# Kernel tuning notes

Hardware: AMD Instinct MI355X
Metric: run time of the kernel (lower is better)

The kernel has to match this reference:

```python
import jax, jax.numpy as jnp
import numpy as np

C_M, C_Z, C = 256, 128, 32
N_SEQ, N_RES = 128, 256


def setup_inputs() -> dict:
    key = jax.random.key(0)
    ks = jax.random.split(key, 9)
    s = 0.02
    return {
        "m": jax.random.normal(ks[0], (N_SEQ, N_RES, C_M), dtype=jnp.float32),
        "ln_w": jnp.ones((C_M,), dtype=jnp.float32),
        "ln_b": jnp.zeros((C_M,), dtype=jnp.float32),
        "w1": jax.random.normal(ks[1], (C, C_M), dtype=jnp.float32) * s,
        "b1": jnp.zeros((C,), dtype=jnp.float32),
        "w2": jax.random.normal(ks[2], (C, C_M), dtype=jnp.float32) * s,
        "b2": jnp.zeros((C,), dtype=jnp.float32),
        "wo": jax.random.normal(ks[3], (C_Z, C * C), dtype=jnp.float32) * s,
        "bo": jnp.zeros((C_Z,), dtype=jnp.float32),
    }


def reference(m, ln_w, ln_b, w1, b1, w2, b2, wo, bo):
    n_seq = m.shape[-3]
    # LayerNorm over c_m
    mu = jnp.mean(m, axis=-1, keepdims=True)
    var = jnp.mean(jnp.square(m - mu), axis=-1, keepdims=True)
    mn = (m - mu) * jax.lax.rsqrt(var + 1e-5) * ln_w + ln_b
    # dual projections to c channels: [s, i, c]
    a = jnp.einsum('sim,cm->sic', mn, w1) + b1
    b = jnp.einsum('sjm,dm->sjd', mn, w2) + b2
    # outer product mean contracted over sequence axis: [i, j, c, d]
    o = jnp.einsum('sic,sjd->ijcd', a, b)
    o = o.reshape(o.shape[0], o.shape[1], C * C)
    # output projection and mean over sequences
    z = (jnp.einsum('ijk,zk->ijz', o, wo) + bo) / n_seq
    return z
```

## Files before the change

### kernel.cpp

```cpp
#include <hip/hip_runtime.h>
#include <hip/hip_bf16.h>
#include <stdint.h>

#define N_RES 256
#define CMDIM 256

typedef __attribute__((ext_vector_type(8))) short bf16x8;
typedef __attribute__((ext_vector_type(4))) float f32x4;
typedef __attribute__((ext_vector_type(2))) unsigned int u32x2;

__device__ __forceinline__ unsigned short f32_to_bf16(float f) {
    union { float f; unsigned int u; } v; v.f = f;
    unsigned int u = v.u;
    return (unsigned short)((u + 0x7FFFu + ((u >> 16) & 1u)) >> 16);
}


__global__ __launch_bounds__(256) void k_prep(
    const float* __restrict__ w1, const float* __restrict__ w2,
    const float* __restrict__ wo,
    unsigned short* __restrict__ Wbf, unsigned short* __restrict__ wof)
{
    int t = blockIdx.x * 256 + threadIdx.x;
    if (t < 16384) {
        int ch = t >> 8, cm = t & 255;
        float v = (ch < 32) ? w1[ch * 256 + cm] : w2[(ch - 32) * 256 + cm];
        int addr = ((ch >> 4) * 8 + (cm >> 5)) * 512 + ((cm >> 3) & 3) * 128 + (ch & 15) * 8 + (cm & 7);
        Wbf[addr] = f32_to_bf16(v);
    }
    if (t < 131072) {
        int zo = t >> 10, k = t & 1023;
        int addr = ((zo >> 4) * 32 + (k >> 5)) * 512 + ((k >> 3) & 3) * 128 + (zo & 15) * 8 + (k & 7);
        wof[addr] = f32_to_bf16(wo[t]);
    }
}

__global__ __launch_bounds__(256) void k_ln_proj(
    const float* __restrict__ m, const float* __restrict__ lnw, const float* __restrict__ lnb,
    const float* __restrict__ b1, const float* __restrict__ b2,
    const unsigned short* __restrict__ Wbf,
    unsigned short* __restrict__ A2f, unsigned short* __restrict__ B2f)
{
    __shared__ unsigned short mn[32 * 256];
    __shared__ unsigned short stg[2048];
    int b = blockIdx.x;
    int i = b >> 2, sblk = b & 3;
    int tid = threadIdx.x;
    int wv = tid >> 6, lane = tid & 63;
    int quad = lane >> 4, l15 = lane & 15;

    f32x4 lw = *(const f32x4*)(lnw + lane * 4);
    f32x4 lb = *(const f32x4*)(lnb + lane * 4);

    #pragma unroll
    for (int r = 0; r < 8; ++r) {
        int sl = wv * 8 + r;
        int s = sblk * 32 + sl;
        const float* row = m + ((size_t)s * N_RES + i) * CMDIM;
        f32x4 x = *(const f32x4*)(row + lane * 4);
        float s1 = x[0] + x[1] + x[2] + x[3];
        float s2 = x[0]*x[0] + x[1]*x[1] + x[2]*x[2] + x[3]*x[3];
        #pragma unroll
        for (int off = 32; off; off >>= 1) {
            s1 += __shfl_xor(s1, off);
            s2 += __shfl_xor(s2, off);
        }
        float mu = s1 * (1.0f / 256.0f);
        float var = s2 * (1.0f / 256.0f) - mu * mu;
        float rstd = rsqrtf(var + 1e-5f);
        float n0 = (x[0] - mu) * rstd * lw[0] + lb[0];
        float n1 = (x[1] - mu) * rstd * lw[1] + lb[1];
        float n2 = (x[2] - mu) * rstd * lw[2] + lb[2];
        float n3 = (x[3] - mu) * rstd * lw[3] + lb[3];
        unsigned int p0 = (unsigned)f32_to_bf16(n0) | ((unsigned)f32_to_bf16(n1) << 16);
        unsigned int p1 = (unsigned)f32_to_bf16(n2) | ((unsigned)f32_to_bf16(n3) << 16);
        int chunk = lane >> 1;
        int pos = (chunk & 16) | ((chunk ^ sl) & 15);
        unsigned int* dst = (unsigned int*)((char*)mn + sl * 512 + pos * 16 + (lane & 1) * 8);
        dst[0] = p0; dst[1] = p1;
    }
    __syncthreads();

    bf16x8 af[8];
    #pragma unroll
    for (int ks = 0; ks < 8; ++ks)
        af[ks] = *(const bf16x8*)(Wbf + (wv * 8 + ks) * 512 + lane * 8);

    f32x4 acc[2];
    acc[0] = (f32x4){0.f, 0.f, 0.f, 0.f};
    acc[1] = (f32x4){0.f, 0.f, 0.f, 0.f};
    #pragma unroll
    for (int ks = 0; ks < 8; ++ks) {
        #pragma unroll
        for (int nb = 0; nb < 2; ++nb) {
            int sl = nb * 16 + l15;
            int chunk = ks * 4 + quad;
            int pos = (chunk & 16) | ((chunk ^ sl) & 15);
            bf16x8 bf = *(const bf16x8*)((char*)mn + sl * 512 + pos * 16);
            acc[nb] = __builtin_amdgcn_mfma_f32_16x16x32_bf16(af[ks], bf, acc[nb], 0, 0, 0);
        }
    }

    const float* bsrc = (wv < 2) ? b1 : b2;
    f32x4 bias = *(const f32x4*)(bsrc + (wv & 1) * 16 + quad * 4);
    unsigned short* sbase = stg + (wv >> 1) * 1024 + (wv & 1) * 512 + quad * 32;
    #pragma unroll
    for (int nb = 0; nb < 2; ++nb) {
        int sl = nb * 16 + l15;
        int soff = ((sl >> 3) & 3) * 128 + (sl & 7);
        #pragma unroll
        for (int reg = 0; reg < 4; ++reg)
            sbase[soff + reg * 8] = f32_to_bf16(acc[nb][reg] + bias[reg]);
    }
    __syncthreads();

    int part = tid >> 7, blk = (tid >> 6) & 1, l = tid & 63;
    unsigned short* gdst = (part ? B2f : A2f) + ((i * 2 + blk) * 4 + sblk) * 512 + l * 8;
    *(bf16x8*)gdst = *(const bf16x8*)(stg + tid * 8);
}

__global__ __launch_bounds__(256, 2) void k_fused(
    const unsigned short* __restrict__ A2f, const unsigned short* __restrict__ B2f,
    const unsigned short* __restrict__ wof, const float* __restrict__ bo,
    float* __restrict__ out)
{
    __shared__ char olds[65536];
    int bx = blockIdx.x;
    int by = blockIdx.y;
    int tid = threadIdx.x, wv = tid >> 6, lane = tid & 63;
    int quad = lane >> 4, l15 = lane & 15;
    int wm = wv & 1, wn = wv >> 1;

    bf16x8 bn[4][4];
    #pragma unroll
    for (int ks = 0; ks < 4; ++ks)
        #pragma unroll
        for (int nb = 0; nb < 4; ++nb)
            bn[ks][nb] = *(const bf16x8*)(A2f + (size_t)(((bx * 8 + wn * 4 + nb) * 4 + ks) * 512) + lane * 8);

    #pragma unroll
    for (int pass = 0; pass < 2; ++pass) {
        f32x4 acc[4][4];
        #pragma unroll
        for (int a = 0; a < 4; ++a)
            #pragma unroll
            for (int b = 0; b < 4; ++b) acc[a][b] = (f32x4){0.f, 0.f, 0.f, 0.f};

        bf16x8 amC[4], amN[4];
        #pragma unroll
        for (int mb = 0; mb < 4; ++mb)
            amC[mb] = *(const bf16x8*)(B2f + (size_t)(((by * 16 + pass * 8 + wm * 4 + mb) * 4 + 0) * 512) + lane * 8);

        #pragma unroll
        for (int ks = 0; ks < 4; ++ks) {
            if (ks < 3) {
                #pragma unroll
                for (int mb = 0; mb < 4; ++mb)
                    amN[mb] = *(const bf16x8*)(B2f + (size_t)(((by * 16 + pass * 8 + wm * 4 + mb) * 4 + ks + 1) * 512) + lane * 8);
            }
            #pragma unroll
            for (int mb = 0; mb < 4; ++mb)
                #pragma unroll
                for (int nb = 0; nb < 4; ++nb)
                    acc[mb][nb] = __builtin_amdgcn_mfma_f32_16x16x32_bf16(amC[mb], bn[ks][nb], acc[mb][nb], 0, 0, 0);
            #pragma unroll
            for (int mb = 0; mb < 4; ++mb) amC[mb] = amN[mb];
        }

        #pragma unroll
        for (int mb = 0; mb < 4; ++mb) {
            int m_ = wm * 64 + mb * 16 + quad * 4;
            int d0 = m_ & 31;
            int jl = pass * 4 + (m_ >> 5);
            #pragma unroll
            for (int nb = 0; nb < 4; ++nb) {
                int n_ = wn * 64 + nb * 16 + l15;
                int c = n_ & 31, il = n_ >> 5;
                int pair = il * 8 + jl;
                int e0 = c * 32 + d0;
                int chunk = e0 >> 3;
                int phys = pair ^ (chunk & 31);
                f32x4 a4 = acc[mb][nb];
                unsigned int p0 = (unsigned)f32_to_bf16(a4[0]) | ((unsigned)f32_to_bf16(a4[1]) << 16);
                unsigned int p1 = (unsigned)f32_to_bf16(a4[2]) | ((unsigned)f32_to_bf16(a4[3]) << 16);
                u32x2 pv = {p0, p1};
                *(u32x2*)(olds + chunk * 512 + phys * 16 + (e0 & 7) * 2) = pv;
            }
        }
    }
    __syncthreads();

    f32x4 acc2[2][2];
    #pragma unroll
    for (int a = 0; a < 2; ++a)
        #pragma unroll
        for (int b = 0; b < 2; ++b) acc2[a][b] = (f32x4){0.f, 0.f, 0.f, 0.f};

    const unsigned short* wbase = wof + (size_t)(wv * 2 * 32) * 512 + lane * 8;

    bf16x8 af[4][2], bfr[4][2];
    #pragma unroll
    for (int p = 0; p < 3; ++p) {
        #pragma unroll
        for (int zb = 0; zb < 2; ++zb)
            af[p][zb] = *(const bf16x8*)(wbase + (size_t)(zb * 32 + p) * 512);
        #pragma unroll
        for (int pb = 0; pb < 2; ++pb) {
            int pair = pb * 16 + l15;
            int chunk = p * 4 + quad;
            int phys = pair ^ (chunk & 31);
            bfr[p][pb] = *(const bf16x8*)(olds + chunk * 512 + phys * 16);
        }
    }

    #pragma unroll
    for (int kt = 0; kt < 32; ++kt) {
        int slot = kt & 3;
        if (kt + 3 < 32) {
            int pf = kt + 3, ps = pf & 3;
            #pragma unroll
            for (int zb = 0; zb < 2; ++zb)
                af[ps][zb] = *(const bf16x8*)(wbase + (size_t)(zb * 32 + pf) * 512);
            #pragma unroll
            for (int pb = 0; pb < 2; ++pb) {
                int pair = pb * 16 + l15;
                int chunk = pf * 4 + quad;
                int phys = pair ^ (chunk & 31);
                bfr[ps][pb] = *(const bf16x8*)(olds + chunk * 512 + phys * 16);
            }
        }
        #pragma unroll
        for (int zb = 0; zb < 2; ++zb)
            #pragma unroll
            for (int pb = 0; pb < 2; ++pb)
                acc2[zb][pb] = __builtin_amdgcn_mfma_f32_16x16x32_bf16(af[slot][zb], bfr[slot][pb], acc2[zb][pb], 0, 0, 0);
    }

    #pragma unroll
    for (int zb = 0; zb < 2; ++zb) {
        int zo = wv * 32 + zb * 16 + quad * 4;
        f32x4 b4 = *(const f32x4*)(bo + zo);
        #pragma unroll
        for (int pb = 0; pb < 2; ++pb) {
            int pair = pb * 16 + l15;
            int i = bx * 4 + (pair >> 3);
            int j = by * 8 + (pair & 7);
            f32x4 v;
            #pragma unroll
            for (int reg = 0; reg < 4; ++reg)
                v[reg] = (acc2[zb][pb][reg] + b4[reg]) * (1.0f / 128.0f);
            *(f32x4*)(out + ((size_t)(i * 256 + j)) * 128 + zo) = v;
        }
    }
}

extern "C" void kernel_launch(void* const* d_in, const int* in_sizes, int n_in,
                              void* d_out, int out_size, void* d_ws, size_t ws_size,
                              hipStream_t stream) {
    const float* m   = (const float*)d_in[0];
    const float* lnw = (const float*)d_in[1];
    const float* lnb = (const float*)d_in[2];
    const float* w1  = (const float*)d_in[3];
    const float* b1  = (const float*)d_in[4];
    const float* w2  = (const float*)d_in[5];
    const float* b2  = (const float*)d_in[6];
    const float* wo  = (const float*)d_in[7];
    const float* bo  = (const float*)d_in[8];
    float* out = (float*)d_out;
    char* ws = (char*)d_ws;

    unsigned short* Wbf = (unsigned short*)(ws);
    unsigned short* wof = (unsigned short*)(ws + 32768);
    unsigned short* A2f = (unsigned short*)(ws + 32768 + 262144);
    unsigned short* B2f = (unsigned short*)(ws + 32768 + 262144 + 2097152);

    hipLaunchKernelGGL(k_prep, dim3(512), dim3(256), 0, stream, w1, w2, wo, Wbf, wof);
    hipLaunchKernelGGL(k_ln_proj, dim3(1024), dim3(256), 0, stream,
                       m, lnw, lnb, b1, b2, Wbf, A2f, B2f);
    hipLaunchKernelGGL(k_fused, dim3(64, 32), dim3(256), 0, stream,
                       A2f, B2f, wof, bo, out);
}
```

Measured before the change: 139.0 us.

## Double fused tile to 8x8 residue pairs with 512-thread blocks

The fused outer-product plus projection kernel now processes 64 (i,j) pairs per block (8 i by 8 j) using 8 waves and 128KB of LDS, instead of 32 pairs with 4 waves. The first GEMM is done in a single pass with 8x4 MFMA tiles per wave, and weight prefetch for the output projection is hoisted above the barrier. This halves the grid and gives better reuse of A/B fragments and wo loads per block. In exchange, occupancy drops to one block per CU because of the LDS size, and register pressure rises from the 32 accumulators.

```diff
diff --git a/kernel.cpp b/kernel.cpp
--- a/kernel.cpp
+++ b/kernel.cpp
@@ -119,99 +119,104 @@
     *(bf16x8*)gdst = *(const bf16x8*)(stg + tid * 8);
 }
 
-__global__ __launch_bounds__(256, 2) void k_fused(
+__global__ __launch_bounds__(512) void k_fused(
     const unsigned short* __restrict__ A2f, const unsigned short* __restrict__ B2f,
     const unsigned short* __restrict__ wof, const float* __restrict__ bo,
     float* __restrict__ out)
 {
-    __shared__ char olds[65536];
+    __shared__ char olds[131072];
     int bx = blockIdx.x;
     int by = blockIdx.y;
     int tid = threadIdx.x, wv = tid >> 6, lane = tid & 63;
     int quad = lane >> 4, l15 = lane & 15;
-    int wm = wv & 1, wn = wv >> 1;
-
-    bf16x8 bn[4][4];
-    #pragma unroll
-    for (int ks = 0; ks < 4; ++ks)
-        #pragma unroll
-        for (int nb = 0; nb < 4; ++nb)
-            bn[ks][nb] = *(const bf16x8*)(A2f + (size_t)(((bx * 8 + wn * 4 + nb) * 4 + ks) * 512) + lane * 8);
-
-    #pragma unroll
-    for (int pass = 0; pass < 2; ++pass) {
-        f32x4 acc[4][4];
-        #pragma unroll
-        for (int a = 0; a < 4; ++a)
-            #pragma unroll
-            for (int b = 0; b < 4; ++b) acc[a][b] = (f32x4){0.f, 0.f, 0.f, 0.f};
-
-        bf16x8 amC[4], amN[4];
-        #pragma unroll
-        for (int mb = 0; mb < 4; ++mb)
-            amC[mb] = *(const bf16x8*)(B2f + (size_t)(((by * 16 + pass * 8 + wm * 4 + mb) * 4 + 0) * 512) + lane * 8);
-
-        #pragma unroll
-        for (int ks = 0; ks < 4; ++ks) {
-            if (ks < 3) {
-                #pragma unroll
-                for (int mb = 0; mb < 4; ++mb)
-                    amN[mb] = *(const bf16x8*)(B2f + (size_t)(((by * 16 + pass * 8 + wm * 4 + mb) * 4 + ks + 1) * 512) + lane * 8);
-            }
-            #pragma unroll
-            for (int mb = 0; mb < 4; ++mb)
-                #pragma unroll
-                for (int nb = 0; nb < 4; ++nb)
-                    acc[mb][nb] = __builtin_amdgcn_mfma_f32_16x16x32_bf16(amC[mb], bn[ks][nb], acc[mb][nb], 0, 0, 0);
-            #pragma unroll
-            for (int mb = 0; mb < 4; ++mb) amC[mb] = amN[mb];
-        }
-
-        #pragma unroll
-        for (int mb = 0; mb < 4; ++mb) {
-            int m_ = wm * 64 + mb * 16 + quad * 4;
-            int d0 = m_ & 31;
-            int jl = pass * 4 + (m_ >> 5);
-            #pragma unroll
-            for (int nb = 0; nb < 4; ++nb) {
-                int n_ = wn * 64 + nb * 16 + l15;
-                int c = n_ & 31, il = n_ >> 5;
-                int pair = il * 8 + jl;
-                int e0 = c * 32 + d0;
-                int chunk = e0 >> 3;
-                int phys = pair ^ (chunk & 31);
-                f32x4 a4 = acc[mb][nb];
-                unsigned int p0 = (unsigned)f32_to_bf16(a4[0]) | ((unsigned)f32_to_bf16(a4[1]) << 16);
-                unsigned int p1 = (unsigned)f32_to_bf16(a4[2]) | ((unsigned)f32_to_bf16(a4[3]) << 16);
-                u32x2 pv = {p0, p1};
-                *(u32x2*)(olds + chunk * 512 + phys * 16 + (e0 & 7) * 2) = pv;
-            }
-        }
-    }
+    int wm = wv & 1, wn = wv >> 2 == 0 ? (wv >> 1) : (wv >> 1);
+    wn = wv >> 1;
+
+    const unsigned short* Abase = A2f + (size_t)((bx * 16 + wn * 4) * 4) * 512 + lane * 8;
+    const unsigned short* Bbase = B2f + (size_t)((by * 16 + wm * 8) * 4) * 512 + lane * 8;
+
+    f32x4 acc[8][4];
+    #pragma unroll
+    for (int a = 0; a < 8; ++a)
+        #pragma unroll
+        for (int b = 0; b < 4; ++b) acc[a][b] = (f32x4){0.f, 0.f, 0.f, 0.f};
+
+    bf16x8 amC[8], amN[8], bnC[4], bnN[4];
+    #pragma unroll
+    for (int mb = 0; mb < 8; ++mb)
+        amC[mb] = *(const bf16x8*)(Bbase + (size_t)(mb * 4) * 512);
+    #pragma unroll
+    for (int nb = 0; nb < 4; ++nb)
+        bnC[nb] = *(const bf16x8*)(Abase + (size_t)(nb * 4) * 512);
+
+    #pragma unroll
+    for (int ks = 0; ks < 4; ++ks) {
+        if (ks < 3) {
+            #pragma unroll
+            for (int mb = 0; mb < 8; ++mb)
+                amN[mb] = *(const bf16x8*)(Bbase + (size_t)(mb * 4 + ks + 1) * 512);
+            #pragma unroll
+            for (int nb = 0; nb < 4; ++nb)
+                bnN[nb] = *(const bf16x8*)(Abase + (size_t)(nb * 4 + ks + 1) * 512);
+        }
+        #pragma unroll
+        for (int mb = 0; mb < 8; ++mb)
+            #pragma unroll
+            for (int nb = 0; nb < 4; ++nb)
+                acc[mb][nb] = __builtin_amdgcn_mfma_f32_16x16x32_bf16(amC[mb], bnC[nb], acc[mb][nb], 0, 0, 0);
+        #pragma unroll
+        for (int mb = 0; mb < 8; ++mb) amC[mb] = amN[mb];
+        #pragma unroll
+        for (int nb = 0; nb < 4; ++nb) bnC[nb] = bnN[nb];
+    }
+
+    #pragma unroll
+    for (int mb = 0; mb < 8; ++mb) {
+        int d0 = (mb & 1) * 16 + quad * 4;
+        int jl = wm * 4 + (mb >> 1);
+        #pragma unroll
+        for (int nb = 0; nb < 4; ++nb) {
+            int c = (nb & 1) * 16 + l15;
+            int il = wn * 2 + (nb >> 1);
+            int pair = il * 8 + jl;
+            int e0 = c * 32 + d0;
+            int chunk = e0 >> 3;
+            int phys = pair ^ (chunk & 63);
+            f32x4 a4 = acc[mb][nb];
+            unsigned int p0 = (unsigned)f32_to_bf16(a4[0]) | ((unsigned)f32_to_bf16(a4[1]) << 16);
+            unsigned int p1 = (unsigned)f32_to_bf16(a4[2]) | ((unsigned)f32_to_bf16(a4[3]) << 16);
+            u32x2 pv = {p0, p1};
+            *(u32x2*)(olds + chunk * 1024 + phys * 16 + (quad & 1) * 8) = pv;
+        }
+    }
+
+    int zg = wv >> 1, pg = wv & 1;
+    const unsigned short* wbase = wof + (size_t)(zg * 64) * 512 + lane * 8;
+
+    bf16x8 af2[4][2], bfr[4][2];
+    #pragma unroll
+    for (int p = 0; p < 3; ++p)
+        #pragma unroll
+        for (int zb = 0; zb < 2; ++zb)
+            af2[p][zb] = *(const bf16x8*)(wbase + (size_t)(zb * 32 + p) * 512);
+
     __syncthreads();
 
+    #pragma unroll
+    for (int p = 0; p < 3; ++p)
+        #pragma unroll
+        for (int pb = 0; pb < 2; ++pb) {
+            int pair = pg * 32 + pb * 16 + l15;
+            int chunk = p * 4 + quad;
+            int phys = pair ^ (chunk & 63);
+            bfr[p][pb] = *(const bf16x8*)(olds + chunk * 1024 + phys * 16);
+        }
+
     f32x4 acc2[2][2];
     #pragma unroll
     for (int a = 0; a < 2; ++a)
         #pragma unroll
         for (int b = 0; b < 2; ++b) acc2[a][b] = (f32x4){0.f, 0.f, 0.f, 0.f};
-
-    const unsigned short* wbase = wof + (size_t)(wv * 2 * 32) * 512 + lane * 8;
-
-    bf16x8 af[4][2], bfr[4][2];
-    #pragma unroll
-    for (int p = 0; p < 3; ++p) {
-        #pragma unroll
-        for (int zb = 0; zb < 2; ++zb)
-            af[p][zb] = *(const bf16x8*)(wbase + (size_t)(zb * 32 + p) * 512);
-        #pragma unroll
-        for (int pb = 0; pb < 2; ++pb) {
-            int pair = pb * 16 + l15;
-            int chunk = p * 4 + quad;
-            int phys = pair ^ (chunk & 31);
-            bfr[p][pb] = *(const bf16x8*)(olds + chunk * 512 + phys * 16);
-        }
-    }
 
     #pragma unroll
     for (int kt = 0; kt < 32; ++kt) {
@@ -220,30 +225,30 @@
             int pf = kt + 3, ps = pf & 3;
             #pragma unroll
             for (int zb = 0; zb < 2; ++zb)
-                af[ps][zb] = *(const bf16x8*)(wbase + (size_t)(zb * 32 + pf) * 512);
+                af2[ps][zb] = *(const bf16x8*)(wbase + (size_t)(zb * 32 + pf) * 512);
             #pragma unroll
             for (int pb = 0; pb < 2; ++pb) {
-                int pair = pb * 16 + l15;
+                int pair = pg * 32 + pb * 16 + l15;
                 int chunk = pf * 4 + quad;
-                int phys = pair ^ (chunk & 31);
-                bfr[ps][pb] = *(const bf16x8*)(olds + chunk * 512 + phys * 16);
+                int phys = pair ^ (chunk & 63);
+                bfr[ps][pb] = *(const bf16x8*)(olds + chunk * 1024 + phys * 16);
             }
         }
         #pragma unroll
         for (int zb = 0; zb < 2; ++zb)
             #pragma unroll
             for (int pb = 0; pb < 2; ++pb)
-                acc2[zb][pb] = __builtin_amdgcn_mfma_f32_16x16x32_bf16(af[slot][zb], bfr[slot][pb], acc2[zb][pb], 0, 0, 0);
+                acc2[zb][pb] = __builtin_amdgcn_mfma_f32_16x16x32_bf16(af2[slot][zb], bfr[slot][pb], acc2[zb][pb], 0, 0, 0);
     }
 
     #pragma unroll
     for (int zb = 0; zb < 2; ++zb) {
-        int zo = wv * 32 + zb * 16 + quad * 4;
+        int zo = zg * 32 + zb * 16 + quad * 4;
         f32x4 b4 = *(const f32x4*)(bo + zo);
         #pragma unroll
         for (int pb = 0; pb < 2; ++pb) {
-            int pair = pb * 16 + l15;
-            int i = bx * 4 + (pair >> 3);
+            int pair = pg * 32 + pb * 16 + l15;
+            int i = bx * 8 + (pair >> 3);
             int j = by * 8 + (pair & 7);
             f32x4 v;
             #pragma unroll
@@ -277,6 +282,6 @@
     hipLaunchKernelGGL(k_prep, dim3(512), dim3(256), 0, stream, w1, w2, wo, Wbf, wof);
     hipLaunchKernelGGL(k_ln_proj, dim3(1024), dim3(256), 0, stream,
                        m, lnw, lnb, b1, b2, Wbf, A2f, B2f);
-    hipLaunchKernelGGL(k_fused, dim3(64, 32), dim3(256), 0, stream,
+    hipLaunchKernelGGL(k_fused, dim3(32, 32), dim3(512), 0, stream,
                        A2f, B2f, wof, bo, out);
 }
```

Result: slower. 147.2 us (+5.9%).

## Double fused tile to 8x8 pairs with 512 threads and split-K reduction

Applied to the files above, without the earlier changes.

The fused outer-product and projection kernel now runs 512-thread blocks, each covering 8x8 (i,j) pairs instead of 4x8. The LDS staging buffer doubles to 128KB and uses a new 6-bit swizzle. The output-projection K loop is split between wave pairs, with the partial sums reduced through LDS. A blockIdx remap groups neighbouring tiles for L2 locality. The aim is to halve how often the wo weights are re-read per pair and to raise MFMA reuse, at the cost of lower occupancy from the large LDS footprint and an extra reduction barrier.

```diff
diff --git a/kernel.cpp b/kernel.cpp
--- a/kernel.cpp
+++ b/kernel.cpp
@@ -13,6 +13,10 @@
     union { float f; unsigned int u; } v; v.f = f;
     unsigned int u = v.u;
     return (unsigned short)((u + 0x7FFFu + ((u >> 16) & 1u)) >> 16);
+}
+
+__device__ __forceinline__ int swz6(int x) {
+    return ((x >> 2) & 7) | (((x >> 5) & 1) << 3) | ((x & 3) << 4);
 }
 
 
@@ -119,27 +123,31 @@
     *(bf16x8*)gdst = *(const bf16x8*)(stg + tid * 8);
 }
 
-__global__ __launch_bounds__(256, 2) void k_fused(
+__global__ __launch_bounds__(512, 2) void k_fused(
     const unsigned short* __restrict__ A2f, const unsigned short* __restrict__ B2f,
     const unsigned short* __restrict__ wof, const float* __restrict__ bo,
     float* __restrict__ out)
 {
-    __shared__ char olds[65536];
-    int bx = blockIdx.x;
-    int by = blockIdx.y;
+    __shared__ char olds[131072];
+    int bid = blockIdx.x;
+    int sb = (bid & 7) * 128 + (bid >> 3);
+    int bx = sb & 31, by = sb >> 5;
     int tid = threadIdx.x, wv = tid >> 6, lane = tid & 63;
     int quad = lane >> 4, l15 = lane & 15;
     int wm = wv & 1, wn = wv >> 1;
 
+    const unsigned short* Abase = A2f + (size_t)((bx * 16 + wn * 4) * 4) * 512 + lane * 8;
+
     bf16x8 bn[4][4];
     #pragma unroll
-    for (int ks = 0; ks < 4; ++ks)
-        #pragma unroll
-        for (int nb = 0; nb < 4; ++nb)
-            bn[ks][nb] = *(const bf16x8*)(A2f + (size_t)(((bx * 8 + wn * 4 + nb) * 4 + ks) * 512) + lane * 8);
+    for (int nb = 0; nb < 4; ++nb)
+        #pragma unroll
+        for (int ks = 0; ks < 4; ++ks)
+            bn[ks][nb] = *(const bf16x8*)(Abase + (size_t)(nb * 4 + ks) * 512);
 
     #pragma unroll
     for (int pass = 0; pass < 2; ++pass) {
+        const unsigned short* Bbase = B2f + (size_t)((by * 16 + pass * 8 + wm * 4) * 4) * 512 + lane * 8;
         f32x4 acc[4][4];
         #pragma unroll
         for (int a = 0; a < 4; ++a)
@@ -149,14 +157,14 @@
         bf16x8 amC[4], amN[4];
         #pragma unroll
         for (int mb = 0; mb < 4; ++mb)
-            amC[mb] = *(const bf16x8*)(B2f + (size_t)(((by * 16 + pass * 8 + wm * 4 + mb) * 4 + 0) * 512) + lane * 8);
+            amC[mb] = *(const bf16x8*)(Bbase + (size_t)(mb * 4) * 512);
 
         #pragma unroll
         for (int ks = 0; ks < 4; ++ks) {
             if (ks < 3) {
                 #pragma unroll
                 for (int mb = 0; mb < 4; ++mb)
-                    amN[mb] = *(const bf16x8*)(B2f + (size_t)(((by * 16 + pass * 8 + wm * 4 + mb) * 4 + ks + 1) * 512) + lane * 8);
+                    amN[mb] = *(const bf16x8*)(Bbase + (size_t)(mb * 4 + ks + 1) * 512);
             }
             #pragma unroll
             for (int mb = 0; mb < 4; ++mb)
@@ -179,77 +187,94 @@
                 int pair = il * 8 + jl;
                 int e0 = c * 32 + d0;
                 int chunk = e0 >> 3;
-                int phys = pair ^ (chunk & 31);
+                int phys = pair ^ swz6(chunk & 63);
                 f32x4 a4 = acc[mb][nb];
                 unsigned int p0 = (unsigned)f32_to_bf16(a4[0]) | ((unsigned)f32_to_bf16(a4[1]) << 16);
                 unsigned int p1 = (unsigned)f32_to_bf16(a4[2]) | ((unsigned)f32_to_bf16(a4[3]) << 16);
                 u32x2 pv = {p0, p1};
-                *(u32x2*)(olds + chunk * 512 + phys * 16 + (e0 & 7) * 2) = pv;
+                *(u32x2*)(olds + chunk * 1024 + phys * 16 + (e0 & 7) * 2) = pv;
             }
         }
     }
-    __syncthreads();
-
-    f32x4 acc2[2][2];
+
+    int zg = wv >> 1, kh = wv & 1, kt0 = kh * 16;
+    const unsigned short* wbase = wof + (size_t)(zg * 64) * 512 + lane * 8;
+
+    bf16x8 af2[4][2], bfr[4][4];
+    #pragma unroll
+    for (int p = 0; p < 3; ++p)
+        #pragma unroll
+        for (int zb = 0; zb < 2; ++zb)
+            af2[p][zb] = *(const bf16x8*)(wbase + (size_t)(zb * 32 + kt0 + p) * 512);
+
+    __syncthreads();
+
+    #pragma unroll
+    for (int p = 0; p < 3; ++p)
+        #pragma unroll
+        for (int pb = 0; pb < 4; ++pb) {
+            int pair = pb * 16 + l15;
+            int chunk = (kt0 + p) * 4 + quad;
+            int phys = pair ^ swz6(chunk & 63);
+            bfr[p][pb] = *(const bf16x8*)(olds + chunk * 1024 + phys * 16);
+        }
+
+    f32x4 acc2[2][4];
     #pragma unroll
     for (int a = 0; a < 2; ++a)
         #pragma unroll
-        for (int b = 0; b < 2; ++b) acc2[a][b] = (f32x4){0.f, 0.f, 0.f, 0.f};
-
-    const unsigned short* wbase = wof + (size_t)(wv * 2 * 32) * 512 + lane * 8;
-
-    bf16x8 af[4][2], bfr[4][2];
-    #pragma unroll
-    for (int p = 0; p < 3; ++p) {
-        #pragma unroll
-        for (int zb = 0; zb < 2; ++zb)
-            af[p][zb] = *(const bf16x8*)(wbase + (size_t)(zb * 32 + p) * 512);
-        #pragma unroll
-        for (int pb = 0; pb < 2; ++pb) {
-            int pair = pb * 16 + l15;
-            int chunk = p * 4 + quad;
-            int phys = pair ^ (chunk & 31);
-            bfr[p][pb] = *(const bf16x8*)(olds + chunk * 512 + phys * 16);
-        }
-    }
-
-    #pragma unroll
-    for (int kt = 0; kt < 32; ++kt) {
+        for (int b = 0; b < 4; ++b) acc2[a][b] = (f32x4){0.f, 0.f, 0.f, 0.f};
+
+    #pragma unroll
+    for (int kt = 0; kt < 16; ++kt) {
         int slot = kt & 3;
-        if (kt + 3 < 32) {
-            int pf = kt + 3, ps = pf & 3;
+        if (kt < 13) {
+            int pf = kt0 + kt + 3, ps = (kt + 3) & 3;
             #pragma unroll
             for (int zb = 0; zb < 2; ++zb)
-                af[ps][zb] = *(const bf16x8*)(wbase + (size_t)(zb * 32 + pf) * 512);
-            #pragma unroll
-            for (int pb = 0; pb < 2; ++pb) {
+                af2[ps][zb] = *(const bf16x8*)(wbase + (size_t)(zb * 32 + pf) * 512);
+            #pragma unroll
+            for (int pb = 0; pb < 4; ++pb) {
                 int pair = pb * 16 + l15;
                 int chunk = pf * 4 + quad;
-                int phys = pair ^ (chunk & 31);
-                bfr[ps][pb] = *(const bf16x8*)(olds + chunk * 512 + phys * 16);
+                int phys = pair ^ swz6(chunk & 63);
+                bfr[ps][pb] = *(const bf16x8*)(olds + chunk * 1024 + phys * 16);
             }
         }
         #pragma unroll
         for (int zb = 0; zb < 2; ++zb)
             #pragma unroll
-            for (int pb = 0; pb < 2; ++pb)
-                acc2[zb][pb] = __builtin_amdgcn_mfma_f32_16x16x32_bf16(af[slot][zb], bfr[slot][pb], acc2[zb][pb], 0, 0, 0);
-    }
-
-    #pragma unroll
-    for (int zb = 0; zb < 2; ++zb) {
-        int zo = wv * 32 + zb * 16 + quad * 4;
-        f32x4 b4 = *(const f32x4*)(bo + zo);
-        #pragma unroll
-        for (int pb = 0; pb < 2; ++pb) {
-            int pair = pb * 16 + l15;
-            int i = bx * 4 + (pair >> 3);
-            int j = by * 8 + (pair & 7);
-            f32x4 v;
-            #pragma unroll
-            for (int reg = 0; reg < 4; ++reg)
-                v[reg] = (acc2[zb][pb][reg] + b4[reg]) * (1.0f / 128.0f);
-            *(f32x4*)(out + ((size_t)(i * 256 + j)) * 128 + zo) = v;
+            for (int pb = 0; pb < 4; ++pb)
+                acc2[zb][pb] = __builtin_amdgcn_mfma_f32_16x16x32_bf16(af2[slot][zb], bfr[slot][pb], acc2[zb][pb], 0, 0, 0);
+    }
+
+    __syncthreads();
+    f32x4* red = (f32x4*)olds;
+    if (kh == 1) {
+        #pragma unroll
+        for (int zb = 0; zb < 2; ++zb)
+            #pragma unroll
+            for (int pb = 0; pb < 4; ++pb)
+                red[(((zg * 2 + zb) * 4 + pb) << 6) + quad * 16 + l15] = acc2[zb][pb];
+    }
+    __syncthreads();
+    if (kh == 0) {
+        #pragma unroll
+        for (int zb = 0; zb < 2; ++zb) {
+            int zo = zg * 32 + zb * 16 + quad * 4;
+            f32x4 b4 = *(const f32x4*)(bo + zo);
+            #pragma unroll
+            for (int pb = 0; pb < 4; ++pb) {
+                f32x4 part = red[(((zg * 2 + zb) * 4 + pb) << 6) + quad * 16 + l15];
+                int pair = pb * 16 + l15;
+                int i = bx * 8 + (pair >> 3);
+                int j = by * 8 + (pair & 7);
+                f32x4 v;
+                #pragma unroll
+                for (int reg = 0; reg < 4; ++reg)
+                    v[reg] = (acc2[zb][pb][reg] + part[reg] + b4[reg]) * (1.0f / 128.0f);
+                *(f32x4*)(out + ((size_t)(i * 256 + j)) * 128 + zo) = v;
+            }
         }
     }
 }
@@ -277,6 +302,6 @@
     hipLaunchKernelGGL(k_prep, dim3(512), dim3(256), 0, stream, w1, w2, wo, Wbf, wof);
     hipLaunchKernelGGL(k_ln_proj, dim3(1024), dim3(256), 0, stream,
                        m, lnw, lnb, b1, b2, Wbf, A2f, B2f);
-    hipLaunchKernelGGL(k_fused, dim3(64, 32), dim3(256), 0, stream,
+    hipLaunchKernelGGL(k_fused, dim3(1024), dim3(512), 0, stream,
                        A2f, B2f, wof, bo, out);
 }
```

Measured after the change: 140.2 us. About the same (+0.9%).

## Remap fused-kernel blocks, preload operands, deepen prefetch, add MFMA priority and new swizzle

Applied to the files above, without the earlier changes.

The fused outer-product/projection kernel now uses a 1D grid, remapped so that consecutive blocks are spread across by-rows, likely to group blocks by XCD for better L2 reuse of A/B tiles. All B-operand k-slices are loaded up front instead of double-buffered, and the wo-projection prefetch is issued before the barrier with two k-steps per pipeline slot. s_setprio raises wave priority around the MFMA bursts, and a different XOR swizzle is used for the LDS staging buffer to cut bank conflicts. These changes raise register pressure, which could hurt occupancy under launch_bounds(256,2).

```diff
diff --git a/kernel.cpp b/kernel.cpp
--- a/kernel.cpp
+++ b/kernel.cpp
@@ -13,6 +13,10 @@
     union { float f; unsigned int u; } v; v.f = f;
     unsigned int u = v.u;
     return (unsigned short)((u + 0x7FFFu + ((u >> 16) & 1u)) >> 16);
+}
+
+__device__ __forceinline__ int swz5(int x) {
+    return ((x >> 2) & 7) | (((x >> 5) & 1) << 3) | ((x & 1) << 4);
 }
 
 
@@ -125,47 +129,47 @@
     float* __restrict__ out)
 {
     __shared__ char olds[65536];
-    int bx = blockIdx.x;
-    int by = blockIdx.y;
+    int bid = blockIdx.x;
+    int sb = (bid & 7) * 256 + (bid >> 3);
+    int bx = sb & 63, by = sb >> 6;
     int tid = threadIdx.x, wv = tid >> 6, lane = tid & 63;
     int quad = lane >> 4, l15 = lane & 15;
     int wm = wv & 1, wn = wv >> 1;
 
+    const unsigned short* Abase = A2f + (size_t)((bx * 8 + wn * 4) * 4) * 512 + lane * 8;
+
     bf16x8 bn[4][4];
     #pragma unroll
-    for (int ks = 0; ks < 4; ++ks)
-        #pragma unroll
-        for (int nb = 0; nb < 4; ++nb)
-            bn[ks][nb] = *(const bf16x8*)(A2f + (size_t)(((bx * 8 + wn * 4 + nb) * 4 + ks) * 512) + lane * 8);
+    for (int nb = 0; nb < 4; ++nb)
+        #pragma unroll
+        for (int ks = 0; ks < 4; ++ks)
+            bn[ks][nb] = *(const bf16x8*)(Abase + (size_t)(nb * 4 + ks) * 512);
 
     #pragma unroll
     for (int pass = 0; pass < 2; ++pass) {
+        const unsigned short* Bbase = B2f + (size_t)((by * 16 + pass * 8 + wm * 4) * 4) * 512 + lane * 8;
         f32x4 acc[4][4];
         #pragma unroll
         for (int a = 0; a < 4; ++a)
             #pragma unroll
             for (int b = 0; b < 4; ++b) acc[a][b] = (f32x4){0.f, 0.f, 0.f, 0.f};
 
-        bf16x8 amC[4], amN[4];
+        bf16x8 am[4][4];
         #pragma unroll
         for (int mb = 0; mb < 4; ++mb)
-            amC[mb] = *(const bf16x8*)(B2f + (size_t)(((by * 16 + pass * 8 + wm * 4 + mb) * 4 + 0) * 512) + lane * 8);
-
-        #pragma unroll
-        for (int ks = 0; ks < 4; ++ks) {
-            if (ks < 3) {
-                #pragma unroll
-                for (int mb = 0; mb < 4; ++mb)
-                    amN[mb] = *(const bf16x8*)(B2f + (size_t)(((by * 16 + pass * 8 + wm * 4 + mb) * 4 + ks + 1) * 512) + lane * 8);
-            }
+            #pragma unroll
+            for (int ks = 0; ks < 4; ++ks)
+                am[ks][mb] = *(const bf16x8*)(Bbase + (size_t)(mb * 4 + ks) * 512);
+
+        __builtin_amdgcn_s_setprio(1);
+        #pragma unroll
+        for (int ks = 0; ks < 4; ++ks)
             #pragma unroll
             for (int mb = 0; mb < 4; ++mb)
                 #pragma unroll
                 for (int nb = 0; nb < 4; ++nb)
-                    acc[mb][nb] = __builtin_amdgcn_mfma_f32_16x16x32_bf16(amC[mb], bn[ks][nb], acc[mb][nb], 0, 0, 0);
-            #pragma unroll
-            for (int mb = 0; mb < 4; ++mb) amC[mb] = amN[mb];
-        }
+                    acc[mb][nb] = __builtin_amdgcn_mfma_f32_16x16x32_bf16(am[ks][mb], bn[ks][nb], acc[mb][nb], 0, 0, 0);
+        __builtin_amdgcn_s_setprio(0);
 
         #pragma unroll
         for (int mb = 0; mb < 4; ++mb) {
@@ -179,7 +183,7 @@
                 int pair = il * 8 + jl;
                 int e0 = c * 32 + d0;
                 int chunk = e0 >> 3;
-                int phys = pair ^ (chunk & 31);
+                int phys = pair ^ swz5(chunk);
                 f32x4 a4 = acc[mb][nb];
                 unsigned int p0 = (unsigned)f32_to_bf16(a4[0]) | ((unsigned)f32_to_bf16(a4[1]) << 16);
                 unsigned int p1 = (unsigned)f32_to_bf16(a4[2]) | ((unsigned)f32_to_bf16(a4[3]) << 16);
@@ -188,57 +192,76 @@
             }
         }
     }
+
+    int zg = wv;
+    const unsigned short* wbase = wof + (size_t)(zg * 64) * 512 + lane * 8;
+
+    bf16x8 af2[4][4], bfr2[4][4];
+    #pragma unroll
+    for (int p = 0; p < 3; ++p)
+        #pragma unroll
+        for (int zb = 0; zb < 2; ++zb)
+            #pragma unroll
+            for (int h = 0; h < 2; ++h)
+                af2[p][zb * 2 + h] = *(const bf16x8*)(wbase + (size_t)(zb * 32 + 2 * p + h) * 512);
+
     __syncthreads();
 
+    #pragma unroll
+    for (int p = 0; p < 3; ++p)
+        #pragma unroll
+        for (int pb = 0; pb < 2; ++pb)
+            #pragma unroll
+            for (int h = 0; h < 2; ++h) {
+                int kt = 2 * p + h;
+                int pair = pb * 16 + l15;
+                int chunk = kt * 4 + quad;
+                int phys = pair ^ swz5(chunk);
+                bfr2[p][pb * 2 + h] = *(const bf16x8*)(olds + chunk * 512 + phys * 16);
+            }
+
     f32x4 acc2[2][2];
     #pragma unroll
     for (int a = 0; a < 2; ++a)
         #pragma unroll
         for (int b = 0; b < 2; ++b) acc2[a][b] = (f32x4){0.f, 0.f, 0.f, 0.f};
 
-    const unsigned short* wbase = wof + (size_t)(wv * 2 * 32) * 512 + lane * 8;
-
-    bf16x8 af[4][2], bfr[4][2];
-    #pragma unroll
-    for (int p = 0; p < 3; ++p) {
-        #pragma unroll
-        for (int zb = 0; zb < 2; ++zb)
-            af[p][zb] = *(const bf16x8*)(wbase + (size_t)(zb * 32 + p) * 512);
-        #pragma unroll
-        for (int pb = 0; pb < 2; ++pb) {
-            int pair = pb * 16 + l15;
-            int chunk = p * 4 + quad;
-            int phys = pair ^ (chunk & 31);
-            bfr[p][pb] = *(const bf16x8*)(olds + chunk * 512 + phys * 16);
-        }
-    }
-
-    #pragma unroll
-    for (int kt = 0; kt < 32; ++kt) {
-        int slot = kt & 3;
-        if (kt + 3 < 32) {
-            int pf = kt + 3, ps = pf & 3;
+    #pragma unroll
+    for (int s = 0; s < 16; ++s) {
+        int slot = s & 3;
+        if (s < 13) {
+            int t = s + 3, ps = t & 3;
             #pragma unroll
             for (int zb = 0; zb < 2; ++zb)
-                af[ps][zb] = *(const bf16x8*)(wbase + (size_t)(zb * 32 + pf) * 512);
-            #pragma unroll
-            for (int pb = 0; pb < 2; ++pb) {
-                int pair = pb * 16 + l15;
-                int chunk = pf * 4 + quad;
-                int phys = pair ^ (chunk & 31);
-                bfr[ps][pb] = *(const bf16x8*)(olds + chunk * 512 + phys * 16);
-            }
-        }
-        #pragma unroll
-        for (int zb = 0; zb < 2; ++zb)
+                #pragma unroll
+                for (int h = 0; h < 2; ++h)
+                    af2[ps][zb * 2 + h] = *(const bf16x8*)(wbase + (size_t)(zb * 32 + 2 * t + h) * 512);
             #pragma unroll
             for (int pb = 0; pb < 2; ++pb)
-                acc2[zb][pb] = __builtin_amdgcn_mfma_f32_16x16x32_bf16(af[slot][zb], bfr[slot][pb], acc2[zb][pb], 0, 0, 0);
+                #pragma unroll
+                for (int h = 0; h < 2; ++h) {
+                    int kt = 2 * t + h;
+                    int pair = pb * 16 + l15;
+                    int chunk = kt * 4 + quad;
+                    int phys = pair ^ swz5(chunk);
+                    bfr2[ps][pb * 2 + h] = *(const bf16x8*)(olds + chunk * 512 + phys * 16);
+                }
+        }
+        __builtin_amdgcn_s_setprio(1);
+        #pragma unroll
+        for (int h = 0; h < 2; ++h)
+            #pragma unroll
+            for (int zb = 0; zb < 2; ++zb)
+                #pragma unroll
+                for (int pb = 0; pb < 2; ++pb)
+                    acc2[zb][pb] = __builtin_amdgcn_mfma_f32_16x16x32_bf16(
+                        af2[slot][zb * 2 + h], bfr2[slot][pb * 2 + h], acc2[zb][pb], 0, 0, 0);
+        __builtin_amdgcn_s_setprio(0);
     }
 
     #pragma unroll
     for (int zb = 0; zb < 2; ++zb) {
-        int zo = wv * 32 + zb * 16 + quad * 4;
+        int zo = zg * 32 + zb * 16 + quad * 4;
         f32x4 b4 = *(const f32x4*)(bo + zo);
         #pragma unroll
         for (int pb = 0; pb < 2; ++pb) {
@@ -277,6 +300,6 @@
     hipLaunchKernelGGL(k_prep, dim3(512), dim3(256), 0, stream, w1, w2, wo, Wbf, wof);
     hipLaunchKernelGGL(k_ln_proj, dim3(1024), dim3(256), 0, stream,
                        m, lnw, lnb, b1, b2, Wbf, A2f, B2f);
-    hipLaunchKernelGGL(k_fused, dim3(64, 32), dim3(256), 0, stream,
+    hipLaunchKernelGGL(k_fused, dim3(2048), dim3(256), 0, stream,
                        A2f, B2f, wof, bo, out);
 }
```

Measured after the change: 141.6 us. No clear change (+1.9%).
